# Performance work log

Hardware: AMD Instinct MI355X
Metric: run time of the kernel (lower is better)

## Reference

```python
import jax, jax.numpy as jnp
import numpy as np
from jax import lax

B, T, C_IN, HID, K, HORIZON = 64, 1024, 256, 512, 3, 12
OUT_DIM = HORIZON * 3


def causal_conv(x, w, b, dilation):
    # x: (B, C_in, T), w: (C_out, C_in, K) -> left-padded causal conv == conv+Chomp1d
    pad = (K - 1) * dilation
    y = lax.conv_general_dilated(x, w, window_strides=(1,), padding=[(pad, 0)],
                                 rhs_dilation=(dilation,),
                                 dimension_numbers=('NCH', 'OIH', 'NCH'))
    return y + b[None, :, None]


def setup_inputs() -> dict:
    key = jax.random.key(0)
    ks = jax.random.split(key, 16)
    N = B * T
    x = jax.random.normal(ks[0], (N, C_IN), jnp.float32)
    edge_index = jax.random.randint(ks[1], (2, N), 0, N, dtype=jnp.int64)
    idx = jnp.arange(N, dtype=jnp.int64)
    batch = idx // T          # graph id per node
    node_time = idx % T       # local time per node
    s1 = 1.0 / np.sqrt(C_IN * K)
    s2 = 1.0 / np.sqrt(HID * K)
    sd = 1.0 / np.sqrt(C_IN)
    sf = 1.0 / np.sqrt(HID)
    return {
        'x': x, 'edge_index': edge_index, 'batch': batch, 'node_time': node_time,
        # TemporalBlock 0 (in=C_IN, out=HID, dilation=1)
        'conv1_w0': jax.random.uniform(ks[2], (HID, C_IN, K), jnp.float32, -s1, s1),
        'conv1_b0': jax.random.uniform(ks[3], (HID,), jnp.float32, -s1, s1),
        'conv2_w0': jax.random.uniform(ks[4], (HID, HID, K), jnp.float32, -s2, s2),
        'conv2_b0': jax.random.uniform(ks[5], (HID,), jnp.float32, -s2, s2),
        'down_w0': jax.random.uniform(ks[6], (HID, C_IN, 1), jnp.float32, -sd, sd),
        'down_b0': jax.random.uniform(ks[7], (HID,), jnp.float32, -sd, sd),
        # TemporalBlock 1 (in=HID, out=HID, dilation=2, no downsample)
        'conv1_w1': jax.random.uniform(ks[8], (HID, HID, K), jnp.float32, -s2, s2),
        'conv1_b1': jax.random.uniform(ks[9], (HID,), jnp.float32, -s2, s2),
        'conv2_w1': jax.random.uniform(ks[10], (HID, HID, K), jnp.float32, -s2, s2),
        'conv2_b1': jax.random.uniform(ks[11], (HID,), jnp.float32, -s2, s2),
        # fc
        'fc_w': jax.random.uniform(ks[12], (OUT_DIM, HID), jnp.float32, -sf, sf),
        'fc_b': jax.random.uniform(ks[13], (OUT_DIM,), jnp.float32, -sf, sf),
    }


def reference(x, edge_index, batch, node_time,
              conv1_w0, conv1_b0, conv2_w0, conv2_b0, down_w0, down_b0,
              conv1_w1, conv1_b1, conv2_w1, conv2_b1, fc_w, fc_b):
    # vectorized scatter replacing the per-node Python loop
    x_seq = jnp.zeros((B, T, C_IN), x.dtype).at[batch, node_time].set(x)
    h = x_seq.transpose(0, 2, 1)  # (B, C_IN, T)
    # TemporalBlock 0 (dropout inactive in eval)
    out = jax.nn.relu(causal_conv(h, conv1_w0, conv1_b0, 1))
    out = jax.nn.relu(causal_conv(out, conv2_w0, conv2_b0, 1))
    res = jnp.einsum('bct,oc->bot', h, down_w0[:, :, 0]) + down_b0[None, :, None]
    h = jax.nn.relu(out + res)
    # TemporalBlock 1
    out = jax.nn.relu(causal_conv(h, conv1_w1, conv1_b1, 2))
    out = jax.nn.relu(causal_conv(out, conv2_w1, conv2_b1, 2))
    h = jax.nn.relu(out + h)
    # last timestep -> fc
    return h[:, :, -1] @ fc_w.T + fc_b
```

## Files before the change

### kernel.cpp

```cpp
#include <hip/hip_runtime.h>


#define OUTD 36
#define F4(q) (*(const float4*)(q))

__device__ __forceinline__ float4 relu4(float4 v) {
  v.x = fmaxf(v.x, 0.f); v.y = fmaxf(v.y, 0.f);
  v.z = fmaxf(v.z, 0.f); v.w = fmaxf(v.w, 0.f);
  return v;
}
__device__ __forceinline__ float4 add4(float4 a, float4 b) {
  a.x += b.x; a.y += b.y; a.z += b.z; a.w += b.w;
  return a;
}
__device__ __forceinline__ float4 addc4(float4 a, float c) {
  a.x += c; a.y += c; a.z += c; a.w += c;
  return a;
}

template <int CIN, int TS_N, int TP, int TOUT, int S, int D, int OFF, int TAPS,
          int OCT, int CCH, int NCH, bool SRC_X, int TS_BASE, int TS_STEP>
__device__ __forceinline__ void conv_body(int bx, int by,
                                          const float* __restrict__ src,
                                          const float* __restrict__ w,
                                          float* __restrict__ Pout) {
    const int tid = threadIdx.x, lane = tid & 63, wv = tid >> 6;
    const int oc0 = bx * OCT;
    constexpr int OCR = OCT / 4;
    __shared__ float Als[CCH * TAPS * OCT];
    __shared__ float Bls[CCH * 64 * TP];
    float acc[OCR][TOUT];
#pragma unroll
    for (int i = 0; i < OCR; ++i)
#pragma unroll
        for (int t = 0; t < TOUT; ++t) acc[i][t] = 0.f;

    for (int ch = 0; ch < NCH; ++ch) {
        const int c0 = (by * NCH + ch) * CCH;
        if (ch) __syncthreads();
        for (int idx = tid; idx < OCT * CCH * TAPS; idx += 256) {
            int i = idx / (CCH * TAPS), r = idx % (CCH * TAPS);
            int c = r / TAPS, kk = r % TAPS;
            Als[(c * TAPS + kk) * OCT + i] =
                w[(size_t)(oc0 + i) * (CIN * TAPS) + (c0 + c) * TAPS + kk];
        }
        if constexpr (SRC_X) {
            for (int idx = tid; idx < CCH * TS_N * 64; idx += 256) {
                int c = idx % CCH, rb = idx / CCH;
                int b = rb & 63, u = rb >> 6;
                Bls[(c * 64 + b) * TP + u] =
                    src[((size_t)b * 1024 + 1011 + TS_BASE + TS_STEP * u) * 256 +
                        c0 + c];
            }
        } else {
            const float4* gp = (const float4*)(src + (size_t)c0 * 64 * TP);
            float4* lp = (float4*)Bls;
            for (int idx = tid; idx < CCH * 64 * TP / 4; idx += 256)
                lp[idx] = gp[idx];
        }
        __syncthreads();
        constexpr int NLOAD = (TP % 4 == 0) ? TP : TS_N;
        for (int c = 0; c < CCH; ++c) {
            float bv[NLOAD];
            if constexpr (TP % 4 == 0) {
#pragma unroll
                for (int q = 0; q < TP / 4; ++q)
                    *(float4*)&bv[4 * q] =
                        *(const float4*)&Bls[(c * 64 + lane) * TP + 4 * q];
            } else {
#pragma unroll
                for (int u = 0; u < TS_N; ++u)
                    bv[u] = Bls[(c * 64 + lane) * TP + u];
            }
            float av[TAPS][OCR];
#pragma unroll
            for (int kk = 0; kk < TAPS; ++kk)
#pragma unroll
                for (int j = 0; j < OCR; j += 4)
                    *(float4*)&av[kk][j] =
                        *(const float4*)&Als[(c * TAPS + kk) * OCT + wv * OCR + j];
#pragma unroll
            for (int i = 0; i < OCR; ++i)
#pragma unroll
                for (int t = 0; t < TOUT; ++t)
#pragma unroll
                    for (int kk = 0; kk < TAPS; ++kk)
                        acc[i][t] += av[kk][i] * bv[S * t + D * kk + OFF];
        }
    }
#pragma unroll
    for (int i = 0; i < OCR; ++i)
#pragma unroll
        for (int t = 0; t < TOUT; ++t)
            Pout[(((size_t)by * 512 + oc0 + wv * OCR + i) * TOUT + t) * 64 +
                 lane] = acc[i][t];
}

template <int CIN, int TS_N, int TP, int TOUT, int S, int D, int OFF, int TAPS,
          int OCT, int CCH, int NCH, bool SRC_X, int TS_BASE, int TS_STEP>
__global__ __launch_bounds__(256) void k_conv(const float* __restrict__ src,
                                              const float* __restrict__ w,
                                              float* __restrict__ Pout) {
    conv_body<CIN, TS_N, TP, TOUT, S, D, OFF, TAPS, OCT, CCH, NCH, SRC_X,
              TS_BASE, TS_STEP>(blockIdx.x, blockIdx.y, src, w, Pout);
}

__global__ __launch_bounds__(256) void k_l0dn(const float* __restrict__ x,
                                              const float* __restrict__ w1_0,
                                              const float* __restrict__ wd0,
                                              float* __restrict__ P0,
                                              float* __restrict__ PD) {
    if (blockIdx.x < 256) {
        conv_body<256, 13, 13, 11, 1, 1, 0, 3, 16, 16, 2, true, 0, 1>(
            blockIdx.x >> 3, blockIdx.x & 7, x, w1_0, P0);
    } else {
        const int q = blockIdx.x - 256;
        conv_body<256, 5, 5, 5, 1, 0, 0, 1, 32, 16, 2, true, 4, 2>(
            q >> 3, q & 7, x, wd0, PD);
    }
}

__global__ __launch_bounds__(256) void k_red0(const float* __restrict__ P0,
                                              const float* __restrict__ b1_0,
                                              float* __restrict__ B1) {
    const int oc = blockIdx.x, tid = threadIdx.x;
    __shared__ float Sm[64 * 12];
    for (int i = tid; i < 768; i += 256) Sm[i] = 0.f;
    __syncthreads();
    if (tid < 176) {
        const int t = tid / 16, b4 = (tid % 16) * 4;
        float4 s = make_float4(0.f, 0.f, 0.f, 0.f);
#pragma unroll
        for (int p = 0; p < 8; ++p)
            s = add4(s, F4(P0 + (((size_t)p * 512 + oc) * 11 + t) * 64 + b4));
        s = relu4(addc4(s, b1_0[oc]));
        Sm[(b4 + 0) * 12 + t] = s.x;
        Sm[(b4 + 1) * 12 + t] = s.y;
        Sm[(b4 + 2) * 12 + t] = s.z;
        Sm[(b4 + 3) * 12 + t] = s.w;
    }
    __syncthreads();
    float4* op = (float4*)(B1 + (size_t)oc * 768);
    for (int i = tid; i < 192; i += 256) op[i] = *(const float4*)&Sm[4 * i];
}

__global__ __launch_bounds__(256) void k_red1(const float* __restrict__ P1,
                                              const float* __restrict__ b2_0,
                                              const float* __restrict__ PD,
                                              const float* __restrict__ bd0,
                                              float* __restrict__ H0,
                                              float* __restrict__ H0f) {
    const int oc = blockIdx.x, tid = threadIdx.x;
    __shared__ float Sm[64 * 12];
    for (int i = tid; i < 768; i += 256) Sm[i] = 0.f;
    __syncthreads();
    if (tid < 80) {
        const int t = tid / 16, b4 = (tid % 16) * 4;
        float4 s = make_float4(0.f, 0.f, 0.f, 0.f);
#pragma unroll
        for (int p = 0; p < 16; ++p)
            s = add4(s, F4(P1 + (((size_t)p * 512 + oc) * 5 + t) * 64 + b4));
        s = relu4(addc4(s, b2_0[oc]));
        float4 s2 = make_float4(0.f, 0.f, 0.f, 0.f);
#pragma unroll
        for (int p = 0; p < 8; ++p)
            s2 = add4(s2, F4(PD + (((size_t)p * 512 + oc) * 5 + t) * 64 + b4));
        s = relu4(addc4(add4(s, s2), bd0[oc]));
        Sm[(b4 + 0) * 12 + t] = s.x;
        Sm[(b4 + 1) * 12 + t] = s.y;
        Sm[(b4 + 2) * 12 + t] = s.z;
        Sm[(b4 + 3) * 12 + t] = s.w;
        if (t == 4) *(float4*)&H0f[(size_t)oc * 64 + b4] = s;
    }
    __syncthreads();
    float4* op = (float4*)(H0 + (size_t)oc * 768);
    for (int i = tid; i < 192; i += 256) op[i] = *(const float4*)&Sm[4 * i];
}

__global__ __launch_bounds__(256) void kD(const float* __restrict__ P2,
                                          const float* __restrict__ b1_1,
                                          const float* __restrict__ w2_1,
                                          float* __restrict__ P3) {
  __shared__ float smem[18432];
  const int tid = threadIdx.x, lane = tid & 63, wv = tid >> 6;
  const int ocp = blockIdx.x >> 3, ks = blockIdx.x & 7, oc0 = ocp * 32;
  const int c0 = ks * 64;
  float* Als = smem;
  float* Bls = smem + 6144;
  float acc[8];
#pragma unroll
  for (int i = 0; i < 8; ++i) acc[i] = 0.f;
  for (int idx = tid; idx < 6144; idx += 256) {
    int i = idx / 192, r = idx % 192, c = r / 3, kk = r % 3;
    Als[(c * 3 + kk) * 32 + i] = w2_1[(oc0 + i) * 1536 + (c0 + c) * 3 + kk];
  }
  for (int idx = tid; idx < 3072; idx += 256) {
    int c = idx / 48, r = idx % 48, u = r / 16, b4 = (r & 15) * 4;
    int cc = c0 + c;
    float4 s = {0.f, 0.f, 0.f, 0.f};
#pragma unroll
    for (int p = 0; p < 8; ++p)
      s = add4(s, F4(&P2[((p * 512 + cc) * 3 + u) * 64 + b4]));
    *(float4*)&Bls[(c * 3 + u) * 64 + b4] = relu4(addc4(s, b1_1[cc]));
  }
  __syncthreads();
  for (int c = 0; c < 64; ++c) {
    float bv[3];
#pragma unroll
    for (int u = 0; u < 3; ++u) bv[u] = Bls[(c * 3 + u) * 64 + lane];
    float av[3][8];
#pragma unroll
    for (int kk = 0; kk < 3; ++kk) {
      *(float4*)&av[kk][0] = F4(&Als[(c * 3 + kk) * 32 + wv * 8]);
      *(float4*)&av[kk][4] = F4(&Als[(c * 3 + kk) * 32 + wv * 8 + 4]);
    }
#pragma unroll
    for (int i = 0; i < 8; ++i)
#pragma unroll
      for (int kk = 0; kk < 3; ++kk) acc[i] += av[kk][i] * bv[kk];
  }
#pragma unroll
  for (int i = 0; i < 8; ++i)
    P3[(ks * 512 + oc0 + wv * 8 + i) * 64 + lane] = acc[i];
}

__global__ __launch_bounds__(256) void kE(const float* __restrict__ P3,
                                          const float* __restrict__ b2_1,
                                          const float* __restrict__ H0f,
                                          const float* __restrict__ fcw,
                                          const float* __restrict__ fcb,
                                          float* __restrict__ out) {
  const int j = blockIdx.x, tid = threadIdx.x;
  const int lane = tid & 63, wv = tid >> 6;
  __shared__ float H1s[16384];
  __shared__ float red[4][64];
  float partial = (wv == 0) ? fcb[j] : 0.f;
  for (int half = 0; half < 2; ++half) {
    const int ocbase = half * 256;
    if (half) __syncthreads();
    for (int idx = tid; idx < 4096; idx += 256) {
      int oc_l = idx >> 4, b4 = (idx & 15) * 4;
      int oc = ocbase + oc_l;
      float4 s = {0.f, 0.f, 0.f, 0.f};
#pragma unroll
      for (int p = 0; p < 8; ++p)
        s = add4(s, F4(&P3[(p * 512 + oc) * 64 + b4]));
      s = relu4(addc4(s, b2_1[oc]));
      s = relu4(add4(s, F4(&H0f[(size_t)oc * 64 + b4])));
      *(float4*)&H1s[oc_l * 64 + b4] = s;
    }
    __syncthreads();
#pragma unroll 8
    for (int r = 0; r < 64; ++r) {
      int oc_l = wv * 64 + r;
      partial += fcw[j * 512 + ocbase + oc_l] * H1s[oc_l * 64 + lane];
    }
  }
  red[wv][lane] = partial;
  __syncthreads();
  if (wv == 0)
    out[lane * OUTD + j] =
        red[0][lane] + red[1][lane] + red[2][lane] + red[3][lane];
}

extern "C" void kernel_launch(void* const* d_in, const int* in_sizes, int n_in,
                              void* d_out, int out_size, void* d_ws, size_t ws_size,
                              hipStream_t stream) {
    const float* x    = (const float*)d_in[0];
    const float* w1_0 = (const float*)d_in[4];
    const float* b1_0 = (const float*)d_in[5];
    const float* w2_0 = (const float*)d_in[6];
    const float* b2_0 = (const float*)d_in[7];
    const float* wd0  = (const float*)d_in[8];
    const float* bd0  = (const float*)d_in[9];
    const float* w1_1 = (const float*)d_in[10];
    const float* b1_1 = (const float*)d_in[11];
    const float* w2_1 = (const float*)d_in[12];
    const float* b2_1 = (const float*)d_in[13];
    const float* fcw  = (const float*)d_in[14];
    const float* fcb  = (const float*)d_in[15];
    float* out = (float*)d_out;

    float* P0  = (float*)d_ws;
    float* B1  = P0 + 8 * 512 * 11 * 64;
    float* P1  = B1 + 512 * 64 * 12;
    float* PD  = P1 + 16 * 512 * 5 * 64;
    float* H0  = PD + 8 * 512 * 5 * 64;
    float* P2  = H0 + 512 * 64 * 12;
    float* P3  = P2 + 8 * 512 * 3 * 64;
    float* H0f = P3 + 8 * 512 * 64;

    k_l0dn<<<384, 256, 0, stream>>>(x, w1_0, wd0, P0, PD);
    k_red0<<<512, 256, 0, stream>>>(P0, b1_0, B1);
    k_conv<512, 11, 12, 5, 2, 1, 0, 3, 32, 16, 2, false, 0, 0>
        <<<dim3(16, 16), 256, 0, stream>>>(B1, w2_0, P1);
    k_red1<<<512, 256, 0, stream>>>(P1, b2_0, PD, bd0, H0, H0f);
    k_conv<512, 5, 12, 3, 1, 1, 0, 3, 32, 16, 4, false, 0, 0>
        <<<dim3(16, 8), 256, 0, stream>>>(H0, w1_1, P2);
    kD<<<128, 256, 0, stream>>>(P2, b1_1, w2_1, P3);
    kE<<<OUTD, 256, 0, stream>>>(P3, b2_1, H0f, fcw, fcb, out);
}
```

Before: 121.8 us.

## Fuse all stages into one persistent kernel with atomic grid barriers

Replaces the seven separate stage kernels with a single persistent kernel of 384 blocks that runs each stage in turn. The stages are separated by software grid barriers built from agent-scope atomic counters, which a memset resets before each launch. This removes per-launch overhead and the gaps between dependent kernels. In exchange, all blocks must be co-resident, blocks in the narrow stages sit idle, a shared LDS buffer caps occupancy, and every barrier adds spin-wait cost.

```diff
diff --git a/kernel.cpp b/kernel.cpp
--- a/kernel.cpp
+++ b/kernel.cpp
@@ -2,6 +2,8 @@
 
 
 #define OUTD 36
+#define NB 384
+#define AGT __HIP_MEMORY_SCOPE_AGENT
 #define F4(q) (*(const float4*)(q))
 
 __device__ __forceinline__ float4 relu4(float4 v) {
@@ -16,6 +18,18 @@
 __device__ __forceinline__ float4 addc4(float4 a, float c) {
   a.x += c; a.y += c; a.z += c; a.w += c;
   return a;
+}
+
+__device__ __forceinline__ void gbar(int* cnt) {
+  __syncthreads();
+  if (threadIdx.x == 0) {
+    __threadfence();
+    __hip_atomic_fetch_add(cnt, 1, __ATOMIC_ACQ_REL, AGT);
+    while (__hip_atomic_load(cnt, __ATOMIC_RELAXED, AGT) < NB)
+      __builtin_amdgcn_s_sleep(2);
+    __threadfence();
+  }
+  __syncthreads();
 }
 
 template <int CIN, int TS_N, int TP, int TOUT, int S, int D, int OFF, int TAPS,
@@ -23,12 +37,13 @@
 __device__ __forceinline__ void conv_body(int bx, int by,
                                           const float* __restrict__ src,
                                           const float* __restrict__ w,
-                                          float* __restrict__ Pout) {
+                                          float* __restrict__ Pout,
+                                          float* smem) {
     const int tid = threadIdx.x, lane = tid & 63, wv = tid >> 6;
     const int oc0 = bx * OCT;
     constexpr int OCR = OCT / 4;
-    __shared__ float Als[CCH * TAPS * OCT];
-    __shared__ float Bls[CCH * 64 * TP];
+    float* Als = smem;
+    float* Bls = smem + CCH * TAPS * OCT;
     float acc[OCR][TOUT];
 #pragma unroll
     for (int i = 0; i < OCR; ++i)
@@ -96,35 +111,11 @@
                  lane] = acc[i][t];
 }
 
-template <int CIN, int TS_N, int TP, int TOUT, int S, int D, int OFF, int TAPS,
-          int OCT, int CCH, int NCH, bool SRC_X, int TS_BASE, int TS_STEP>
-__global__ __launch_bounds__(256) void k_conv(const float* __restrict__ src,
-                                              const float* __restrict__ w,
-                                              float* __restrict__ Pout) {
-    conv_body<CIN, TS_N, TP, TOUT, S, D, OFF, TAPS, OCT, CCH, NCH, SRC_X,
-              TS_BASE, TS_STEP>(blockIdx.x, blockIdx.y, src, w, Pout);
-}
-
-__global__ __launch_bounds__(256) void k_l0dn(const float* __restrict__ x,
-                                              const float* __restrict__ w1_0,
-                                              const float* __restrict__ wd0,
-                                              float* __restrict__ P0,
-                                              float* __restrict__ PD) {
-    if (blockIdx.x < 256) {
-        conv_body<256, 13, 13, 11, 1, 1, 0, 3, 16, 16, 2, true, 0, 1>(
-            blockIdx.x >> 3, blockIdx.x & 7, x, w1_0, P0);
-    } else {
-        const int q = blockIdx.x - 256;
-        conv_body<256, 5, 5, 5, 1, 0, 0, 1, 32, 16, 2, true, 4, 2>(
-            q >> 3, q & 7, x, wd0, PD);
-    }
-}
-
-__global__ __launch_bounds__(256) void k_red0(const float* __restrict__ P0,
-                                              const float* __restrict__ b1_0,
-                                              float* __restrict__ B1) {
-    const int oc = blockIdx.x, tid = threadIdx.x;
-    __shared__ float Sm[64 * 12];
+__device__ __forceinline__ void red0_body(int oc, const float* __restrict__ P0,
+                                          const float* __restrict__ b1_0,
+                                          float* __restrict__ B1, float* Sm) {
+    const int tid = threadIdx.x;
+    __syncthreads();
     for (int i = tid; i < 768; i += 256) Sm[i] = 0.f;
     __syncthreads();
     if (tid < 176) {
@@ -144,14 +135,14 @@
     for (int i = tid; i < 192; i += 256) op[i] = *(const float4*)&Sm[4 * i];
 }
 
-__global__ __launch_bounds__(256) void k_red1(const float* __restrict__ P1,
-                                              const float* __restrict__ b2_0,
-                                              const float* __restrict__ PD,
-                                              const float* __restrict__ bd0,
-                                              float* __restrict__ H0,
-                                              float* __restrict__ H0f) {
-    const int oc = blockIdx.x, tid = threadIdx.x;
-    __shared__ float Sm[64 * 12];
+__device__ __forceinline__ void red1_body(int oc, const float* __restrict__ P1,
+                                          const float* __restrict__ b2_0,
+                                          const float* __restrict__ PD,
+                                          const float* __restrict__ bd0,
+                                          float* __restrict__ H0,
+                                          float* __restrict__ H0f, float* Sm) {
+    const int tid = threadIdx.x;
+    __syncthreads();
     for (int i = tid; i < 768; i += 256) Sm[i] = 0.f;
     __syncthreads();
     if (tid < 80) {
@@ -177,13 +168,12 @@
     for (int i = tid; i < 192; i += 256) op[i] = *(const float4*)&Sm[4 * i];
 }
 
-__global__ __launch_bounds__(256) void kD(const float* __restrict__ P2,
-                                          const float* __restrict__ b1_1,
-                                          const float* __restrict__ w2_1,
-                                          float* __restrict__ P3) {
-  __shared__ float smem[18432];
+__device__ __forceinline__ void kD_body(int bid, const float* __restrict__ P2,
+                                        const float* __restrict__ b1_1,
+                                        const float* __restrict__ w2_1,
+                                        float* __restrict__ P3, float* smem) {
   const int tid = threadIdx.x, lane = tid & 63, wv = tid >> 6;
-  const int ocp = blockIdx.x >> 3, ks = blockIdx.x & 7, oc0 = ocp * 32;
+  const int ocp = bid >> 3, ks = bid & 7, oc0 = ocp * 32;
   const int c0 = ks * 64;
   float* Als = smem;
   float* Bls = smem + 6144;
@@ -224,16 +214,15 @@
     P3[(ks * 512 + oc0 + wv * 8 + i) * 64 + lane] = acc[i];
 }
 
-__global__ __launch_bounds__(256) void kE(const float* __restrict__ P3,
-                                          const float* __restrict__ b2_1,
-                                          const float* __restrict__ H0f,
-                                          const float* __restrict__ fcw,
-                                          const float* __restrict__ fcb,
-                                          float* __restrict__ out) {
-  const int j = blockIdx.x, tid = threadIdx.x;
-  const int lane = tid & 63, wv = tid >> 6;
-  __shared__ float H1s[16384];
-  __shared__ float red[4][64];
+__device__ __forceinline__ void kE_body(int j, const float* __restrict__ P3,
+                                        const float* __restrict__ b2_1,
+                                        const float* __restrict__ H0f,
+                                        const float* __restrict__ fcw,
+                                        const float* __restrict__ fcb,
+                                        float* __restrict__ out, float* smem) {
+  const int tid = threadIdx.x, lane = tid & 63, wv = tid >> 6;
+  float* H1s = smem;
+  float* red = smem + 16384;
   float partial = (wv == 0) ? fcb[j] : 0.f;
   for (int half = 0; half < 2; ++half) {
     const int ocbase = half * 256;
@@ -256,47 +245,92 @@
       partial += fcw[j * 512 + ocbase + oc_l] * H1s[oc_l * 64 + lane];
     }
   }
-  red[wv][lane] = partial;
+  red[wv * 64 + lane] = partial;
   __syncthreads();
   if (wv == 0)
-    out[lane * OUTD + j] =
-        red[0][lane] + red[1][lane] + red[2][lane] + red[3][lane];
+    out[lane * OUTD + j] = red[0 * 64 + lane] + red[1 * 64 + lane] +
+                           red[2 * 64 + lane] + red[3 * 64 + lane];
+}
+
+struct Params {
+  const float* x;
+  const float *w1_0, *b1_0, *w2_0, *b2_0, *wd0, *bd0;
+  const float *w1_1, *b1_1, *w2_1, *b2_1, *fcw, *fcb;
+  float* out;
+  float *P0, *B1, *P1, *PD, *H0, *P2, *P3, *H0f;
+  int* FL;
+};
+
+__global__ __launch_bounds__(256, 2) void mega(Params p) {
+  __shared__ float smem[18688];
+  const int bid = blockIdx.x;
+
+  if (bid < 256) {
+    conv_body<256, 13, 13, 11, 1, 1, 0, 3, 16, 16, 2, true, 0, 1>(
+        bid >> 3, bid & 7, p.x, p.w1_0, p.P0, smem);
+  } else {
+    const int q = bid - 256;
+    conv_body<256, 5, 5, 5, 1, 0, 0, 1, 32, 16, 2, true, 4, 2>(
+        q >> 3, q & 7, p.x, p.wd0, p.PD, smem);
+  }
+  gbar(&p.FL[0]);
+
+  red0_body(bid, p.P0, p.b1_0, p.B1, smem);
+  if (bid < 128) red0_body(bid + 384, p.P0, p.b1_0, p.B1, smem);
+  gbar(&p.FL[1]);
+
+  if (bid < 256)
+    conv_body<512, 11, 12, 5, 2, 1, 0, 3, 32, 16, 2, false, 0, 0>(
+        bid & 15, bid >> 4, p.B1, p.w2_0, p.P1, smem);
+  gbar(&p.FL[2]);
+
+  red1_body(bid, p.P1, p.b2_0, p.PD, p.bd0, p.H0, p.H0f, smem);
+  if (bid < 128)
+    red1_body(bid + 384, p.P1, p.b2_0, p.PD, p.bd0, p.H0, p.H0f, smem);
+  gbar(&p.FL[3]);
+
+  if (bid < 128)
+    conv_body<512, 5, 12, 3, 1, 1, 0, 3, 32, 16, 4, false, 0, 0>(
+        bid & 15, bid >> 4, p.H0, p.w1_1, p.P2, smem);
+  gbar(&p.FL[4]);
+
+  if (bid < 128) kD_body(bid, p.P2, p.b1_1, p.w2_1, p.P3, smem);
+  gbar(&p.FL[5]);
+
+  if (bid < 36)
+    kE_body(bid, p.P3, p.b2_1, p.H0f, p.fcw, p.fcb, p.out, smem);
 }
 
 extern "C" void kernel_launch(void* const* d_in, const int* in_sizes, int n_in,
                               void* d_out, int out_size, void* d_ws, size_t ws_size,
                               hipStream_t stream) {
-    const float* x    = (const float*)d_in[0];
-    const float* w1_0 = (const float*)d_in[4];
-    const float* b1_0 = (const float*)d_in[5];
-    const float* w2_0 = (const float*)d_in[6];
-    const float* b2_0 = (const float*)d_in[7];
-    const float* wd0  = (const float*)d_in[8];
-    const float* bd0  = (const float*)d_in[9];
-    const float* w1_1 = (const float*)d_in[10];
-    const float* b1_1 = (const float*)d_in[11];
-    const float* w2_1 = (const float*)d_in[12];
-    const float* b2_1 = (const float*)d_in[13];
-    const float* fcw  = (const float*)d_in[14];
-    const float* fcb  = (const float*)d_in[15];
-    float* out = (float*)d_out;
-
-    float* P0  = (float*)d_ws;
-    float* B1  = P0 + 8 * 512 * 11 * 64;
-    float* P1  = B1 + 512 * 64 * 12;
-    float* PD  = P1 + 16 * 512 * 5 * 64;
-    float* H0  = PD + 8 * 512 * 5 * 64;
-    float* P2  = H0 + 512 * 64 * 12;
-    float* P3  = P2 + 8 * 512 * 3 * 64;
-    float* H0f = P3 + 8 * 512 * 64;
-
-    k_l0dn<<<384, 256, 0, stream>>>(x, w1_0, wd0, P0, PD);
-    k_red0<<<512, 256, 0, stream>>>(P0, b1_0, B1);
-    k_conv<512, 11, 12, 5, 2, 1, 0, 3, 32, 16, 2, false, 0, 0>
-        <<<dim3(16, 16), 256, 0, stream>>>(B1, w2_0, P1);
-    k_red1<<<512, 256, 0, stream>>>(P1, b2_0, PD, bd0, H0, H0f);
-    k_conv<512, 5, 12, 3, 1, 1, 0, 3, 32, 16, 4, false, 0, 0>
-        <<<dim3(16, 8), 256, 0, stream>>>(H0, w1_1, P2);
-    kD<<<128, 256, 0, stream>>>(P2, b1_1, w2_1, P3);
-    kE<<<OUTD, 256, 0, stream>>>(P3, b2_1, H0f, fcw, fcb, out);
-}
+  Params p;
+  p.x    = (const float*)d_in[0];
+  p.w1_0 = (const float*)d_in[4];
+  p.b1_0 = (const float*)d_in[5];
+  p.w2_0 = (const float*)d_in[6];
+  p.b2_0 = (const float*)d_in[7];
+  p.wd0  = (const float*)d_in[8];
+  p.bd0  = (const float*)d_in[9];
+  p.w1_1 = (const float*)d_in[10];
+  p.b1_1 = (const float*)d_in[11];
+  p.w2_1 = (const float*)d_in[12];
+  p.b2_1 = (const float*)d_in[13];
+  p.fcw  = (const float*)d_in[14];
+  p.fcb  = (const float*)d_in[15];
+  p.out  = (float*)d_out;
+
+  float* base = (float*)d_ws;
+  p.P0  = base;
+  p.B1  = p.P0 + 2883584;
+  p.P1  = p.B1 + 393216;
+  p.PD  = p.P1 + 2621440;
+  p.H0  = p.PD + 1310720;
+  p.P2  = p.H0 + 393216;
+  p.P3  = p.P2 + 786432;
+  p.H0f = p.P3 + 262144;
+  p.FL  = (int*)(p.H0f + 32768);
+
+  hipMemsetAsync((void*)p.FL, 0, 6 * sizeof(int), stream);
+  mega<<<NB, 256, 0, stream>>>(p);
+}
```

Result: slower. 389.3 us (+219.6%).
